# Optimization experiments

Measured on AMD Instinct MI355X. Metric: run time of the kernel, lower is better.

Reference implementation:

```python
import jax, jax.numpy as jnp
import numpy as np

NUM_EMBEDDINGS = 4096
EMBEDDING_DIM = 512
N_TOKENS = 32768
COMMITMENT_COST = 0.25


def setup_inputs() -> dict:
    key = jax.random.key(0)
    k1, k2 = jax.random.split(key)
    flat_input = jax.random.normal(k1, (N_TOKENS, EMBEDDING_DIM), dtype=jnp.float32)
    # torch init: uniform(-1/K, 1/K)
    weight = jax.random.uniform(k2, (NUM_EMBEDDINGS, EMBEDDING_DIM), dtype=jnp.float32,
                                minval=-1.0 / NUM_EMBEDDINGS, maxval=1.0 / NUM_EMBEDDINGS)
    return {"flat_input": flat_input, "weight": weight}


def reference(flat_input, weight):
    distances = (jnp.sum(flat_input ** 2, axis=1, keepdims=True)
                 + jnp.sum(weight ** 2, axis=1)
                 - 2.0 * jnp.matmul(flat_input, weight.T))
    encoding_indices = jnp.argmin(distances, axis=1)  # [N]
    # one-hot @ weight == direct gather of codebook rows
    quantized = weight[encoding_indices]  # [N, D]

    e_latent_loss = jnp.mean((jax.lax.stop_gradient(quantized) - flat_input) ** 2, axis=1)
    q_latent_loss = jnp.mean((quantized - jax.lax.stop_gradient(flat_input)) ** 2, axis=1)
    loss = q_latent_loss + COMMITMENT_COST * e_latent_loss  # [N]

    # straight-through estimator
    quantized_st = flat_input + jax.lax.stop_gradient(quantized - flat_input)

    # avg_probs = mean of one-hot encodings over batch = normalized code counts
    counts = jnp.zeros((NUM_EMBEDDINGS,), dtype=flat_input.dtype).at[encoding_indices].add(1.0)
    avg_probs = counts / flat_input.shape[0]
    perplexity = jnp.exp(-jnp.sum(avg_probs * jnp.log(avg_probs + 1e-10)))

    return quantized_st, loss, perplexity, encoding_indices
```

## Files before the change

### kernel.cpp

```cpp
#include <hip/hip_runtime.h>
#include <math.h>

#define N_TOK 32768
#define K_CODES 4096
#define DIM 512
#define COMMIT 0.25f
#define NCAND 8
#define NSPLIT 2
#define SPLIT_CODES (K_CODES / NSPLIT)
#define NITER (SPLIT_CODES / 256)
#define BIAS 0.125f

typedef short s16x8 __attribute__((ext_vector_type(8)));
typedef float f32x4 __attribute__((ext_vector_type(4)));
typedef unsigned int uint32;
typedef unsigned long long u64;
typedef unsigned short u16;

__device__ __forceinline__ u16 f2bf(float f) {
    uint32 b = __float_as_uint(f);
    return (u16)((b + 0x7FFFu + ((b >> 16) & 1u)) >> 16);
}

__device__ __forceinline__ void gload16(const u16* g, u16* l) {
    __builtin_amdgcn_global_load_lds(
        (const __attribute__((address_space(1))) void*)g,
        (__attribute__((address_space(3))) void*)l,
        16, 0, 0);
}

__global__ __launch_bounds__(256) void tobf16_kernel(const float* __restrict__ src,
                                                     u16* __restrict__ dst, int n4) {
    int i = blockIdx.x * 256 + threadIdx.x;
    int stride = gridDim.x * 256;
    for (; i < n4; i += stride) {
        float4 v = ((const float4*)src)[i];
        ushort4 o;
        o.x = f2bf(v.x); o.y = f2bf(v.y); o.z = f2bf(v.z); o.w = f2bf(v.w);
        ((ushort4*)dst)[i] = o;
    }
}

__global__ __launch_bounds__(256) void rowsq_np_kernel(const float* __restrict__ a,
                                                       float* __restrict__ out,
                                                       int nrows) {
    #pragma clang fp contract(off)
    const int gw   = (blockIdx.x * 256 + threadIdx.x) >> 6;
    const int lane = threadIdx.x & 63;
    const int row  = gw * 8 + (lane >> 3);
    const int j    = lane & 7;
    if (row >= nrows) return;
    const float* p = a + (size_t)row * DIM;
    float blk[4];
    #pragma unroll
    for (int b = 0; b < 4; ++b) {
        const float* q = p + b * 128;
        float v = q[j];
        float r = v * v;
        for (int i = 8; i < 128; i += 8) { float u = q[i + j]; r += u * u; }
        float s1 = r  + __shfl_xor(r, 1);
        float s2 = s1 + __shfl_xor(s1, 2);
        float s3 = s2 + __shfl_xor(s2, 4);
        blk[b] = s3;
    }
    float res = (blk[0] + blk[1]) + (blk[2] + blk[3]);
    if (j == 0) out[row] = res;
}

__global__ __launch_bounds__(512, 2) void screen_kernel(const u16* __restrict__ xb,
                                                        const u16* __restrict__ wb,
                                                        const float* __restrict__ w2f,
                                                        u64* __restrict__ candPart) {
    __shared__ __attribute__((aligned(16))) u16 POOL[77824];

    const int tid  = threadIdx.x;
    const int wv   = tid >> 6;
    const int wt   = wv >> 2;
    const int wc   = wv & 3;
    const int lane = tid & 63;
    const int quad = lane >> 4;
    const int n15  = lane & 15;
    const int m0   = blockIdx.x * 128;
    const int sbase = blockIdx.y * SPLIT_CODES;

    const int l8  = lane >> 3;
    const int qsw = (lane & 7) ^ l8;

    const u16* xg0 = xb + (size_t)(m0 + wv * 16 + l8) * DIM + qsw * 8;
    const u16* xg1 = xg0 + (size_t)8 * DIM;
    const u16* wg0 = wb + (size_t)(sbase + wv * 32 + 0  + l8) * DIM + qsw * 8;
    const u16* wg1 = wg0 + (size_t)8 * DIM;
    const u16* wg2 = wg0 + (size_t)16 * DIM;
    const u16* wg3 = wg0 + (size_t)24 * DIM;

    {
        float* w2l = (float*)&POOL[73728];
        for (int i = tid; i < SPLIT_CODES; i += 512)
            w2l[i] = w2f[sbase + i] + BIAS;
    }

    uint32 r1[16], r2[16];
    #pragma unroll
    for (int i = 0; i < 16; ++i) { r1[i] = 0xFFFFFFFFu; r2[i] = 0xFFFFFFFFu; }

    f32x4 acc[4][4];
    #pragma unroll
    for (int i = 0; i < 4; ++i)
        #pragma unroll
        for (int c = 0; c < 4; ++c) acc[i][c] = (f32x4){0.f, 0.f, 0.f, 0.f};

    #pragma unroll
    for (int tt = 0; tt < 2; ++tt) {
        const int ko = tt * 64;
        gload16(xg0 + ko, &POOL[tt * 8192 + wv * 1024]);
        gload16(xg1 + ko, &POOL[tt * 8192 + wv * 1024 + 512]);
        gload16(wg0 + ko, &POOL[24576 + tt * 16384 + wv * 2048]);
        gload16(wg1 + ko, &POOL[24576 + tt * 16384 + wv * 2048 + 512]);
        gload16(wg2 + ko, &POOL[24576 + tt * 16384 + wv * 2048 + 1024]);
        gload16(wg3 + ko, &POOL[24576 + tt * 16384 + wv * 2048 + 1536]);
    }
    __syncthreads();

    int bufc = 0;
    for (int t = 0; t < 64; ++t) {
        if (t < 63) asm volatile("s_waitcnt vmcnt(6)" ::: "memory");
        else        asm volatile("s_waitcnt vmcnt(0)" ::: "memory");
        __builtin_amdgcn_s_barrier();
        __builtin_amdgcn_sched_barrier(0);

        if (t <= 61) {
            const int bn  = (bufc == 0) ? 2 : bufc - 1;
            const int tn  = t + 2;
            const size_t co = (size_t)(tn >> 3) * (256 * DIM) + (tn & 7) * 64;
            const int ko  = (tn & 7) * 64;
            const size_t xo = (size_t)ko;
            gload16(xg0 + xo, &POOL[bn * 8192 + wv * 1024]);
            gload16(xg1 + xo, &POOL[bn * 8192 + wv * 1024 + 512]);
            gload16(wg0 + co, &POOL[24576 + bn * 16384 + wv * 2048]);
            gload16(wg1 + co, &POOL[24576 + bn * 16384 + wv * 2048 + 512]);
            gload16(wg2 + co, &POOL[24576 + bn * 16384 + wv * 2048 + 1024]);
            gload16(wg3 + co, &POOL[24576 + bn * 16384 + wv * 2048 + 1536]);
        }

        {
            const u16* X = &POOL[bufc * 8192];
            const u16* W = &POOL[24576 + bufc * 16384];
            #pragma unroll
            for (int s = 0; s < 2; ++s) {
                const int lq = s * 4 + quad;
                s16x8 af[4], bf[4];
                #pragma unroll
                for (int i = 0; i < 4; ++i) {
                    const int tr = wt * 64 + i * 16 + n15;
                    af[i] = *(const s16x8*)&X[tr * 64 + (lq ^ (tr & 7)) * 8];
                }
                #pragma unroll
                for (int c = 0; c < 4; ++c) {
                    const int cr = wc * 64 + c * 16 + n15;
                    bf[c] = *(const s16x8*)&W[cr * 64 + (lq ^ (cr & 7)) * 8];
                }
                #pragma unroll
                for (int i = 0; i < 4; ++i)
                    #pragma unroll
                    for (int c = 0; c < 4; ++c)
                        acc[i][c] = __builtin_amdgcn_mfma_f32_16x16x32_bf16(af[i], bf[c], acc[i][c], 0, 0, 0);
            }
        }

        if ((t & 7) == 7) {
            const int it = t >> 3;
            const float* w2l = (const float*)&POOL[73728];
            float w2pb[4];
            #pragma unroll
            for (int c = 0; c < 4; ++c)
                w2pb[c] = w2l[it * 256 + wc * 64 + c * 16 + n15];
            #pragma unroll
            for (int i = 0; i < 4; ++i)
                #pragma unroll
                for (int r = 0; r < 4; ++r) {
                    const int ti = i * 4 + r;
                    #pragma unroll
                    for (int c = 0; c < 4; ++c) {
                        float s = fmaf(-2.0f, acc[i][c][r], w2pb[c]);
                        uint32 key = (__float_as_uint(s) & 0xFFFFFFC0u) | (uint32)((it << 2) | c);
                        uint32 mx = r1[ti] > key ? r1[ti] : key;
                        r1[ti] = r1[ti] < key ? r1[ti] : key;
                        r2[ti] = r2[ti] < mx ? r2[ti] : mx;
                    }
                }
            #pragma unroll
            for (int i = 0; i < 4; ++i)
                #pragma unroll
                for (int c = 0; c < 4; ++c) acc[i][c] = (f32x4){0.f, 0.f, 0.f, 0.f};
        }

        bufc = (bufc == 2) ? 0 : bufc + 1;
    }

    u64* MS = (u64*)POOL;
    for (int phase = 0; phase < 2; ++phase) {
        __syncthreads();
        if (wt == phase) {
            #pragma unroll
            for (int ti = 0; ti < 16; ++ti) {
                const int i = ti >> 2, r = ti & 3;
                const int tloc = i * 16 + quad * 4 + r;
                #pragma unroll
                for (int e = 0; e < 2; ++e) {
                    uint32 k  = e ? r2[ti] : r1[ti];
                    uint32 vb = k & 0xFFFFFFC0u;
                    uint32 id = k & 63u;
                    uint32 code = (uint32)(sbase + (id >> 2) * 256 + wc * 64 + (id & 3) * 16 + n15);
                    MS[tloc * 128 + (wc * 16 + n15) * 2 + e] = ((u64)vb << 32) | code;
                }
            }
        }
        __syncthreads();
        if (tid < 64) {
            u64 best[6];
            #pragma unroll
            for (int c = 0; c < 6; ++c) best[c] = 0xFFFFFFFFFFFFFFFFull;
            for (int e = 0; e < 128; ++e) {
                u64 v = MS[tid * 128 + e];
                if (v < best[5]) {
                    best[5] = v;
                    #pragma unroll
                    for (int p = 5; p > 0; --p)
                        if (best[p] < best[p - 1]) { u64 tv = best[p]; best[p] = best[p - 1]; best[p - 1] = tv; }
                }
            }
            const int token = m0 + phase * 64 + tid;
            u64* dst = candPart + ((size_t)blockIdx.y * N_TOK + token) * 6;
            #pragma unroll
            for (int c = 0; c < 6; ++c) dst[c] = best[c];
        }
    }
}

__global__ __launch_bounds__(256) void mergecand_kernel(const u64* __restrict__ candPart,
                                                        int* __restrict__ candF) {
    int t = blockIdx.x * 256 + threadIdx.x;
    u64 best[NCAND];
    #pragma unroll
    for (int c = 0; c < NCAND; ++c) best[c] = 0xFFFFFFFFFFFFFFFFull;
    for (int s = 0; s < NSPLIT; ++s) {
        const u64* src = candPart + ((size_t)s * N_TOK + t) * 6;
        #pragma unroll
        for (int c = 0; c < 6; ++c) {
            u64 v = src[c];
            if (v < best[NCAND - 1]) {
                best[NCAND - 1] = v;
                #pragma unroll
                for (int p = NCAND - 1; p > 0; --p)
                    if (best[p] < best[p - 1]) { u64 tv = best[p]; best[p] = best[p - 1]; best[p - 1] = tv; }
            }
        }
    }
    #pragma unroll
    for (int c = 0; c < NCAND; ++c) candF[(size_t)t * NCAND + c] = (int)(best[c] & 0xFFFu);
}

__global__ __launch_bounds__(256) void refine_kernel(const float* __restrict__ x,
                                                     const float* __restrict__ w,
                                                     const float* __restrict__ x2np,
                                                     const float* __restrict__ w2np,
                                                     const int* __restrict__ cand,
                                                     int* __restrict__ idx) {
    const int t    = blockIdx.x * 4 + (threadIdx.x >> 6);
    const int lane = threadIdx.x & 63;

    const float* xr = x + (size_t)t * DIM;
    float xv[8];
    #pragma unroll
    for (int j = 0; j < 8; ++j) xv[j] = xr[lane + 64 * j];
    const float x2 = x2np[t];

    float bd = 3.4e38f;
    int   bk = 0x7fffffff;
    for (int c = 0; c < NCAND; ++c) {
        int k = cand[(size_t)t * NCAND + c];
        const float* wr = w + (size_t)k * DIM;
        double m = 0.0;
        #pragma unroll
        for (int j = 0; j < 8; ++j)
            m = fma((double)xv[j], (double)wr[lane + 64 * j], m);
        #pragma unroll
        for (int off = 32; off >= 1; off >>= 1) m += __shfl_down(m, off);
        if (lane == 0) {
            #pragma clang fp contract(off)
            float m32 = (float)m;
            float T1  = x2 + w2np[k];
            float d   = T1 - 2.0f * m32;
            if (d < bd || (d == bd && k < bk)) { bd = d; bk = k; }
        }
    }
    if (lane == 0) idx[t] = bk;
}

__global__ __launch_bounds__(256) void gather_kernel(const float* __restrict__ x,
                                                     const float* __restrict__ w,
                                                     const int* __restrict__ idx,
                                                     float* __restrict__ out_q,
                                                     float* __restrict__ out_loss,
                                                     float* __restrict__ out_ind,
                                                     int* __restrict__ counts) {
    const int wave = threadIdx.x >> 6;
    const int lane = threadIdx.x & 63;
    const int token = blockIdx.x * 4 + wave;
    const int k = idx[token];

    const float4* xr = (const float4*)(x + (size_t)token * DIM);
    const float4* wr = (const float4*)(w + (size_t)k * DIM);
    float4*       qo = (float4*)(out_q + (size_t)token * DIM);

    float ss = 0.f;
    #pragma unroll
    for (int j = 0; j < 2; ++j) {
        int e = lane + j * 64;
        float4 xv = xr[e];
        float4 wv = wr[e];
        float4 d, o;
        d.x = wv.x - xv.x; o.x = xv.x + d.x;
        d.y = wv.y - xv.y; o.y = xv.y + d.y;
        d.z = wv.z - xv.z; o.z = xv.z + d.z;
        d.w = wv.w - xv.w; o.w = xv.w + d.w;
        ss += d.x * d.x + d.y * d.y + d.z * d.z + d.w * d.w;
        qo[e] = o;
    }
    #pragma unroll
    for (int off = 32; off >= 1; off >>= 1) ss += __shfl_down(ss, off);
    if (lane == 0) {
        float lm = ss * (1.0f / DIM);
        out_loss[token] = lm + COMMIT * lm;
        out_ind[token] = (float)k;
        atomicAdd(&counts[k], 1);
    }
}

__global__ __launch_bounds__(256) void perplex_kernel(const int* __restrict__ counts,
                                                      float* __restrict__ out2) {
    __shared__ double red[4];
    const int tid = threadIdx.x;
    const int lane = tid & 63;
    const int wid = tid >> 6;
    double s = 0.0;
    for (int t = tid; t < K_CODES; t += 256) {
        int c = counts[t];
        if (c) {
            double p = (double)c * (1.0 / N_TOK);
            s += p * log(p + 1e-10);
        }
    }
    #pragma unroll
    for (int off = 32; off >= 1; off >>= 1) s += __shfl_down(s, off);
    if (lane == 0) red[wid] = s;
    __syncthreads();
    if (tid == 0) {
        double t = red[0] + red[1] + red[2] + red[3];
        out2[0] = (float)exp(-t);
    }
}

extern "C" void kernel_launch(void* const* d_in, const int* in_sizes, int n_in,
                              void* d_out, int out_size, void* d_ws, size_t ws_size,
                              hipStream_t stream) {
    const float* x = (const float*)d_in[0];
    const float* w = (const float*)d_in[1];

    float* out0 = (float*)d_out;
    float* out1 = out0 + (size_t)N_TOK * DIM;
    float* out2 = out1 + N_TOK;
    float* out3 = out2 + 1;

    u64*   candPart = (u64*)d_ws;
    float* x2np     = (float*)(candPart + (size_t)NSPLIT * N_TOK * 6);
    float* w2np     = x2np + N_TOK;
    int*   idx      = (int*)(w2np + K_CODES);
    int*   counts   = idx + N_TOK;
    int*   candF    = counts + K_CODES;
    u16*   x_bf     = (u16*)(candF + (size_t)N_TOK * NCAND);
    u16*   w_bf     = x_bf + (size_t)N_TOK * DIM;

    hipMemsetAsync(counts, 0, K_CODES * sizeof(int), stream);

    tobf16_kernel<<<4096, 256, 0, stream>>>(x, x_bf, N_TOK * DIM / 4);
    tobf16_kernel<<<2048, 256, 0, stream>>>(w, w_bf, K_CODES * DIM / 4);
    rowsq_np_kernel<<<N_TOK / 32, 256, 0, stream>>>(x, x2np, N_TOK);
    rowsq_np_kernel<<<K_CODES / 32, 256, 0, stream>>>(w, w2np, K_CODES);
    screen_kernel<<<dim3(N_TOK / 128, NSPLIT), 512, 0, stream>>>(x_bf, w_bf, w2np, candPart);
    mergecand_kernel<<<N_TOK / 256, 256, 0, stream>>>(candPart, candF);
    refine_kernel<<<N_TOK / 4, 256, 0, stream>>>(x, w, x2np, w2np, candF, idx);
    gather_kernel<<<N_TOK / 4, 256, 0, stream>>>(x, w, idx, out0, out1, out3, counts);
    perplex_kernel<<<1, 256, 0, stream>>>(counts, out2);
}
```

Before: 446.9 us.

## Double-buffer LDS fragments in registers and relax occupancy bound in screen kernel

The MFMA main loop now preloads the first k-half of A/B fragments for the next tile into registers while the current tile's second half is consumed, so LDS reads overlap with MFMA issue. LDS swizzled offsets are precomputed once outside the loop. Launch bounds drop from 2 to 1 blocks per CU, giving more registers for the extra fragment buffers. The hand-tuned vmcnt(6) wait plus raw barrier is replaced with __syncthreads, which may wait on all outstanding global loads and shorten the global prefetch overlap.

```diff
diff --git a/kernel.cpp b/kernel.cpp
--- a/kernel.cpp
+++ b/kernel.cpp
@@ -67,7 +67,7 @@
     if (j == 0) out[row] = res;
 }
 
-__global__ __launch_bounds__(512, 2) void screen_kernel(const u16* __restrict__ xb,
+__global__ __launch_bounds__(512, 1) void screen_kernel(const u16* __restrict__ xb,
                                                         const u16* __restrict__ wb,
                                                         const float* __restrict__ w2f,
                                                         u64* __restrict__ candPart) {
@@ -109,6 +109,20 @@
         #pragma unroll
         for (int c = 0; c < 4; ++c) acc[i][c] = (f32x4){0.f, 0.f, 0.f, 0.f};
 
+    int xoff0[4], woff0[4], xoff1[4], woff1[4];
+    #pragma unroll
+    for (int i = 0; i < 4; ++i) {
+        const int tr = wt * 64 + i * 16 + n15;
+        xoff0[i] = tr * 64 + ((quad)     ^ (tr & 7)) * 8;
+        xoff1[i] = tr * 64 + ((4 + quad) ^ (tr & 7)) * 8;
+    }
+    #pragma unroll
+    for (int c = 0; c < 4; ++c) {
+        const int cr = wc * 64 + c * 16 + n15;
+        woff0[c] = cr * 64 + ((quad)     ^ (cr & 7)) * 8;
+        woff1[c] = cr * 64 + ((4 + quad) ^ (cr & 7)) * 8;
+    }
+
     #pragma unroll
     for (int tt = 0; tt < 2; ++tt) {
         const int ko = tt * 64;
@@ -121,19 +135,21 @@
     }
     __syncthreads();
 
+    s16x8 pa[4], pb[4];
+    #pragma unroll
+    for (int i = 0; i < 4; ++i) pa[i] = *(const s16x8*)&POOL[xoff0[i]];
+    #pragma unroll
+    for (int c = 0; c < 4; ++c) pb[c] = *(const s16x8*)&POOL[24576 + woff0[c]];
+
     int bufc = 0;
     for (int t = 0; t < 64; ++t) {
-        if (t < 63) asm volatile("s_waitcnt vmcnt(6)" ::: "memory");
-        else        asm volatile("s_waitcnt vmcnt(0)" ::: "memory");
-        __builtin_amdgcn_s_barrier();
-        __builtin_amdgcn_sched_barrier(0);
+        __syncthreads();
 
         if (t <= 61) {
             const int bn  = (bufc == 0) ? 2 : bufc - 1;
             const int tn  = t + 2;
             const size_t co = (size_t)(tn >> 3) * (256 * DIM) + (tn & 7) * 64;
-            const int ko  = (tn & 7) * 64;
-            const size_t xo = (size_t)ko;
+            const size_t xo = (size_t)((tn & 7) * 64);
             gload16(xg0 + xo, &POOL[bn * 8192 + wv * 1024]);
             gload16(xg1 + xo, &POOL[bn * 8192 + wv * 1024 + 512]);
             gload16(wg0 + co, &POOL[24576 + bn * 16384 + wv * 2048]);
@@ -142,30 +158,36 @@
             gload16(wg3 + co, &POOL[24576 + bn * 16384 + wv * 2048 + 1536]);
         }
 
-        {
-            const u16* X = &POOL[bufc * 8192];
-            const u16* W = &POOL[24576 + bufc * 16384];
-            #pragma unroll
-            for (int s = 0; s < 2; ++s) {
-                const int lq = s * 4 + quad;
-                s16x8 af[4], bf[4];
-                #pragma unroll
-                for (int i = 0; i < 4; ++i) {
-                    const int tr = wt * 64 + i * 16 + n15;
-                    af[i] = *(const s16x8*)&X[tr * 64 + (lq ^ (tr & 7)) * 8];
-                }
-                #pragma unroll
-                for (int c = 0; c < 4; ++c) {
-                    const int cr = wc * 64 + c * 16 + n15;
-                    bf[c] = *(const s16x8*)&W[cr * 64 + (lq ^ (cr & 7)) * 8];
-                }
-                #pragma unroll
-                for (int i = 0; i < 4; ++i)
-                    #pragma unroll
-                    for (int c = 0; c < 4; ++c)
-                        acc[i][c] = __builtin_amdgcn_mfma_f32_16x16x32_bf16(af[i], bf[c], acc[i][c], 0, 0, 0);
-            }
-        }
+        const u16* X = &POOL[bufc * 8192];
+        const u16* W = &POOL[24576 + bufc * 16384];
+
+        s16x8 qa[4], qb[4];
+        #pragma unroll
+        for (int i = 0; i < 4; ++i) qa[i] = *(const s16x8*)&X[xoff1[i]];
+        #pragma unroll
+        for (int c = 0; c < 4; ++c) qb[c] = *(const s16x8*)&W[woff1[c]];
+
+        #pragma unroll
+        for (int i = 0; i < 4; ++i)
+            #pragma unroll
+            for (int c = 0; c < 4; ++c)
+                acc[i][c] = __builtin_amdgcn_mfma_f32_16x16x32_bf16(pa[i], pb[c], acc[i][c], 0, 0, 0);
+
+        if (t < 63) {
+            const int bn1 = (bufc == 2) ? 0 : bufc + 1;
+            const u16* Xn = &POOL[bn1 * 8192];
+            const u16* Wn = &POOL[24576 + bn1 * 16384];
+            #pragma unroll
+            for (int i = 0; i < 4; ++i) pa[i] = *(const s16x8*)&Xn[xoff0[i]];
+            #pragma unroll
+            for (int c = 0; c < 4; ++c) pb[c] = *(const s16x8*)&Wn[woff0[c]];
+        }
+
+        #pragma unroll
+        for (int i = 0; i < 4; ++i)
+            #pragma unroll
+            for (int c = 0; c < 4; ++c)
+                acc[i][c] = __builtin_amdgcn_mfma_f32_16x16x32_bf16(qa[i], qb[c], acc[i][c], 0, 0, 0);
 
         if ((t & 7) == 7) {
             const int it = t >> 3;
```

After: 439.3 us. Within noise of the previous version (-1.7%).
